# Kernel optimization log

Hardware: AMD Instinct MI355X
Metric: run time of the kernel (lower is better)

The kernel has to match this reference:

```python
import jax, jax.numpy as jnp
import numpy as np

D_K = 64
NEG_INF = -1.0e9

def setup_inputs() -> dict:
    key = jax.random.key(0)
    kq, kk, kv, km = jax.random.split(key, 4)
    B, H, S, D = 2, 16, 2048, D_K
    Q = jax.random.normal(kq, (B, H, S, D), dtype=jnp.float32)
    K = jax.random.normal(kk, (B, H, S, D), dtype=jnp.float32)
    V = jax.random.normal(kv, (B, H, S, D), dtype=jnp.float32)
    # True entries are masked out (torch masked_fill semantics)
    attn_mask = jax.random.randint(km, (B, H, S, S), 0, 2).astype(jnp.bool_)
    return {"Q": Q, "K": K, "V": V, "attn_mask": attn_mask}

def reference(Q, K, V, attn_mask):
    # scores: [B, H, len_q, len_k]
    scale = 1.0 / np.sqrt(D_K).astype(np.float32)
    scores = jnp.einsum('bhqd,bhkd->bhqk', Q, K) * scale
    scores = jnp.where(attn_mask, jnp.float32(NEG_INF), scores)
    attn = jax.nn.softmax(scores, axis=-1)
    prob = jnp.einsum('bhqk,bhkd->bhqd', attn, V)
    return (prob, attn)
```

## Files before the change

### kernel.cpp

```cpp
#include <hip/hip_runtime.h>
#include <hip/hip_bf16.h>

#define S_LEN 2048
#define D_DIM 64
#define QT    64
#define KT    64
#define NTHR  256
#define NKT   (S_LEN / KT)
#define NBLK  1024
#define PROB_ELEMS 4194304LL

typedef float        f32x4  __attribute__((ext_vector_type(4)));
typedef int          i32x4  __attribute__((ext_vector_type(4)));
typedef unsigned int u32x4  __attribute__((ext_vector_type(4)));
typedef short        bf16x8 __attribute__((ext_vector_type(8)));

__device__ __forceinline__ unsigned short f2bf(float f) {
    return __builtin_bit_cast(unsigned short, __float2bfloat16(f));
}
__device__ __forceinline__ int swzc(int row, int ch) {
    return ch ^ ((row ^ (row >> 3)) & 7);
}
__device__ __forceinline__ float4 scale4(float4 v, float s) {
    v.x *= s; v.y *= s; v.z *= s; v.w *= s; return v;
}
__device__ __forceinline__ u32x4 packbf(float4 a, float4 b) {
    u32x4 r;
    r[0] = (unsigned)f2bf(a.x) | ((unsigned)f2bf(a.y) << 16);
    r[1] = (unsigned)f2bf(a.z) | ((unsigned)f2bf(a.w) << 16);
    r[2] = (unsigned)f2bf(b.x) | ((unsigned)f2bf(b.y) << 16);
    r[3] = (unsigned)f2bf(b.z) | ((unsigned)f2bf(b.w) << 16);
    return r;
}
__device__ __forceinline__ unsigned cvtpk(float lo, float hi) {
    unsigned r;
    asm("v_cvt_pk_bf16_f32 %0, %1, %2" : "=v"(r) : "v"(lo), "v"(hi));
    return r;
}
__device__ __forceinline__ void glds16(const unsigned* g, unsigned char* l) {
    __builtin_amdgcn_global_load_lds(
        (const __attribute__((address_space(1))) unsigned*)g,
        (__attribute__((address_space(3))) unsigned*)(void*)l, 16, 0, 0);
}

__global__ void mask_probe_kernel(const unsigned int* __restrict__ m,
                                  int* __restrict__ flag) {
    unsigned int v = m[threadIdx.x];
    unsigned long long ok = __ballot(v <= 1u);
    if (threadIdx.x == 0) *flag = (ok == ~0ULL) ? 1 : 0;
}

#define KPART 524288
#define VPART 65536
__global__ __launch_bounds__(256)
void kv_prep(const float* __restrict__ Kg, const float* __restrict__ Vg,
             unsigned* __restrict__ Kbf, unsigned* __restrict__ Vtb) {
    int tid = blockIdx.x * 256 + threadIdx.x;
    if (tid < KPART) {
        int ch = tid & 7, rowg = tid >> 3;
        const float* src = Kg + (long long)rowg * D_DIM + ch * 8;
        float4 a = *(const float4*)src, b = *(const float4*)(src + 4);
        int bh = rowg >> 11, k = rowg & 2047, kt = k >> 6, row = k & 63;
        unsigned* dst = Kbf + ((unsigned)(bh * NKT + kt) << 11)
                            + row * 32 + swzc(row, ch) * 4;
        *(u32x4*)dst = packbf(a, b);
    } else if (tid < KPART + VPART) {
        int idx = tid - KPART;
        int d = idx & 63, kt = (idx >> 6) & 31, bh = idx >> 11;
        const float* vb = Vg + (long long)(bh * S_LEN + kt * KT) * D_DIM + d;
        unsigned* tile = Vtb + ((unsigned)(bh * NKT + kt) << 11) + d * 32;
        #pragma unroll
        for (int ci = 0; ci < 8; ++ci) {
            u32x4 o;
            #pragma unroll
            for (int s = 0; s < 4; ++s) {
                float lo = vb[(ci * 8 + 2 * s) * D_DIM];
                float hi = vb[(ci * 8 + 2 * s + 1) * D_DIM];
                o[s] = (unsigned)f2bf(lo) | ((unsigned)f2bf(hi) << 16);
            }
            *(u32x4*)(tile + swzc(d, ci) * 4) = o;
        }
    }
}


#define LOAD_MBITS(DST, KTV)                                                \
    { unsigned bz = 0u;                                                     \
      _Pragma("unroll")                                                     \
      for (int n = 0; n < 4; ++n) {                                         \
        unsigned idx = rowoff + (unsigned)((KTV) * KT + n * 16 + 4 * g);    \
        if (mask32) {                                                       \
            i32x4 m4 = *(const i32x4*)(((const int*)maskB) + idx);          \
            bz |= ((m4[0] ? 1u : 0u) | (m4[1] ? 2u : 0u) |                  \
                   (m4[2] ? 4u : 0u) | (m4[3] ? 8u : 0u)) << (n * 4);       \
        } else {                                                            \
            unsigned mb = *(const unsigned*)(maskB + idx);                  \
            bz |= (((mb & 0xffu) ? 1u : 0u) | ((mb & 0xff00u) ? 2u : 0u) |  \
                   ((mb & 0xff0000u) ? 4u : 0u) |                           \
                   ((mb & 0xff000000u) ? 8u : 0u)) << (n * 4);              \
        } }                                                                 \
      (DST) = bz; }

#define LOAD_BITS2(DST, KTV)                                                \
    { if (useWS) (DST) = (unsigned)bitsWS[bitbase + (unsigned)(KTV) * NTHR];\
      else LOAD_MBITS(DST, KTV) }

#define PH1_TILE(KS, BITS)                                                  \
    { unsigned bb = (BITS);                                                 \
      _Pragma("unroll")                                                     \
      for (int n = 0; n < 4; ++n) {                                         \
        int rowk = n * 16 + c;                                              \
        bf16x8 kf0 = *(const bf16x8*)((KS) + rowk * 128 + swzc(rowk, g) * 16);     \
        bf16x8 kf1 = *(const bf16x8*)((KS) + rowk * 128 + swzc(rowk, 4 + g) * 16); \
        f32x4 acc = {0.f, 0.f, 0.f, 0.f};                                   \
        acc = __builtin_amdgcn_mfma_f32_16x16x32_bf16(kf0, qf0, acc, 0, 0, 0); \
        acc = __builtin_amdgcn_mfma_f32_16x16x32_bf16(kf1, qf1, acc, 0, 0, 0); \
        unsigned mb = bb >> (n * 4);                                        \
        psum += (mb & 1u) ? 0.f : __expf(acc[0]);                           \
        psum += (mb & 2u) ? 0.f : __expf(acc[1]);                           \
        psum += (mb & 4u) ? 0.f : __expf(acc[2]);                           \
        psum += (mb & 8u) ? 0.f : __expf(acc[3]);                           \
      } }

#define PH2_TILE(KS, VT, BITS, KTV)                                         \
    { unsigned bb = (BITS);                                                 \
      _Pragma("unroll")                                                     \
      for (int n = 0; n < 4; ++n) {                                         \
        int rowk = n * 16 + c;                                              \
        bf16x8 kf0 = *(const bf16x8*)((KS) + rowk * 128 + swzc(rowk, g) * 16);     \
        bf16x8 kf1 = *(const bf16x8*)((KS) + rowk * 128 + swzc(rowk, 4 + g) * 16); \
        f32x4 acc = {0.f, 0.f, 0.f, 0.f};                                   \
        acc = __builtin_amdgcn_mfma_f32_16x16x32_bf16(kf0, qf0, acc, 0, 0, 0); \
        acc = __builtin_amdgcn_mfma_f32_16x16x32_bf16(kf1, qf1, acc, 0, 0, 0); \
        unsigned mb = bb >> (n * 4);                                        \
        f32x4 ev;                                                           \
        ev[0] = (mb & 1u) ? 0.f : __expf(acc[0]) * rinv;                    \
        ev[1] = (mb & 2u) ? 0.f : __expf(acc[1]) * rinv;                    \
        ev[2] = (mb & 4u) ? 0.f : __expf(acc[2]) * rinv;                    \
        ev[3] = (mb & 8u) ? 0.f : __expf(acc[3]) * rinv;                    \
        unsigned idx0 = rowoff + (unsigned)((KTV) * KT + n * 16 + 4 * g);   \
        __builtin_nontemporal_store(ev, (f32x4*)(attnOut + idx0));          \
        uint2 pkv; pkv.x = cvtpk(ev[0], ev[1]); pkv.y = cvtpk(ev[2], ev[3]);\
        int kloc = n * 16 + 4 * g;                                          \
        *(uint2*)(Ps + ql * 128 + swzc(ql, kloc >> 3) * 16 + (kloc & 7) * 2) = pkv; \
      }                                                                     \
      { bf16x8 pa0 = *(const bf16x8*)(Ps + ql * 128 + swzc(ql, g) * 16);    \
        bf16x8 pa1 = *(const bf16x8*)(Ps + ql * 128 + swzc(ql, 4 + g) * 16);\
        __builtin_amdgcn_s_setprio(1);                                      \
        _Pragma("unroll")                                                   \
        for (int df = 0; df < 4; ++df) {                                    \
            int d = df * 16 + c;                                            \
            bf16x8 vb0 = *(const bf16x8*)((VT) + d * 128 + swzc(d, g) * 16);     \
            bf16x8 vb1 = *(const bf16x8*)((VT) + d * 128 + swzc(d, 4 + g) * 16); \
            pacc[df] = __builtin_amdgcn_mfma_f32_16x16x32_bf16(pa0, vb0, pacc[df], 0, 0, 0); \
            pacc[df] = __builtin_amdgcn_mfma_f32_16x16x32_bf16(pa1, vb1, pacc[df], 0, 0, 0); \
        }                                                                   \
        __builtin_amdgcn_s_setprio(0); } }

__global__ __launch_bounds__(NTHR, 4)
void attn_fused_glds(const float* __restrict__ Qg,
                     const unsigned* __restrict__ Kbf,
                     const unsigned* __restrict__ Vtb,
                     const unsigned char* __restrict__ maskB,
                     const int* __restrict__ flagp,
                     unsigned short* __restrict__ bitsWS, int useWS,
                     float* __restrict__ attnOut, float* __restrict__ probOut) {
    __shared__ unsigned char sm[40960];
    unsigned char* Ks0 = sm;
    unsigned char* Ks1 = sm + 8192;
    unsigned char* Vt0 = sm + 16384;
    unsigned char* Vt1 = sm + 24576;
    unsigned char* Ps  = sm + 32768;

    const int t = threadIdx.x;
    const int lane = t & 63, w = t >> 6, c = lane & 15, g = lane >> 4;

    const int orig = blockIdx.x;
    const int virt = (orig & 7) * 128 + (orig >> 3);
    const int qt = virt & 31, bh = virt >> 5;
    const int mask32 = *flagp;

    const int qrowbase = bh * S_LEN + qt * QT;
    const int ql = w * 16 + c;
    const unsigned rowoff = (unsigned)(qrowbase + ql) * (unsigned)S_LEN;
    const unsigned bitbase = (unsigned)virt * NKT * NTHR + (unsigned)t;
    const unsigned ktile0 = (unsigned)(bh * NKT) << 11;

    const int f0u = t * 4, f1u = (NTHR + t) * 4;
    const int dst0 = (t & ~63) * 16, dst1 = (NTHR + (t & ~63)) * 16;

    #pragma unroll
    for (int i = 0; i < 2; ++i) {
        int flat = i * NTHR + t, row = flat >> 3, ch = flat & 7;
        const float* src = Qg + (qrowbase + row) * D_DIM + ch * 8;
        float4 a = *(const float4*)src, b = *(const float4*)(src + 4);
        *(u32x4*)(Ps + row * 128 + swzc(row, ch) * 16) =
            packbf(scale4(a, 0.125f), scale4(b, 0.125f));
    }
    __syncthreads();
    bf16x8 qf0 = *(const bf16x8*)(Ps + ql * 128 + swzc(ql, g) * 16);
    bf16x8 qf1 = *(const bf16x8*)(Ps + ql * 128 + swzc(ql, 4 + g) * 16);

    float psum = 0.f;
    unsigned bA, bB;
    {
        const unsigned* kp = Kbf + ktile0;
        glds16(kp + f0u, Ks0 + dst0);
        glds16(kp + f1u, Ks0 + dst1);
    }
    LOAD_MBITS(bA, 0)

    for (int j = 0; j < NKT / 2; ++j) {
        const int ktA = 2 * j, ktB = 2 * j + 1;
        __syncthreads();
        {
            const unsigned* kp = Kbf + ktile0 + (unsigned)ktB * 2048;
            glds16(kp + f0u, Ks1 + dst0);
            glds16(kp + f1u, Ks1 + dst1);
        }
        LOAD_MBITS(bB, ktB)
        PH1_TILE(Ks0, bA)
        if (useWS) bitsWS[bitbase + (unsigned)ktA * NTHR] = (unsigned short)bA;

        __syncthreads();
        if (j + 1 < NKT / 2) {
            const unsigned* kp = Kbf + ktile0 + (unsigned)(ktA + 2) * 2048;
            glds16(kp + f0u, Ks0 + dst0);
            glds16(kp + f1u, Ks0 + dst1);
            LOAD_MBITS(bA, ktA + 2)
        }
        PH1_TILE(Ks1, bB)
        if (useWS) bitsWS[bitbase + (unsigned)ktB * NTHR] = (unsigned short)bB;
    }

    float s = psum;
    s += __shfl_xor(s, 16, 64);
    s += __shfl_xor(s, 32, 64);
    const float rinv = 1.0f / s;

    f32x4 pacc[4];
    #pragma unroll
    for (int d = 0; d < 4; ++d) pacc[d] = (f32x4){0.f, 0.f, 0.f, 0.f};

    {
        const unsigned* kp = Kbf + ktile0;
        const unsigned* vp = Vtb + ktile0;
        glds16(kp + f0u, Ks0 + dst0); glds16(kp + f1u, Ks0 + dst1);
        glds16(vp + f0u, Vt0 + dst0); glds16(vp + f1u, Vt0 + dst1);
    }
    LOAD_BITS2(bA, 0)

    for (int j = 0; j < NKT / 2; ++j) {
        const int ktA = 2 * j, ktB = 2 * j + 1;
        __syncthreads();
        {
            const unsigned* kp = Kbf + ktile0 + (unsigned)ktB * 2048;
            const unsigned* vp = Vtb + ktile0 + (unsigned)ktB * 2048;
            glds16(kp + f0u, Ks1 + dst0); glds16(kp + f1u, Ks1 + dst1);
            glds16(vp + f0u, Vt1 + dst0); glds16(vp + f1u, Vt1 + dst1);
        }
        LOAD_BITS2(bB, ktB)
        PH2_TILE(Ks0, Vt0, bA, ktA)

        __syncthreads();
        if (j + 1 < NKT / 2) {
            const unsigned* kp = Kbf + ktile0 + (unsigned)(ktA + 2) * 2048;
            const unsigned* vp = Vtb + ktile0 + (unsigned)(ktA + 2) * 2048;
            glds16(kp + f0u, Ks0 + dst0); glds16(kp + f1u, Ks0 + dst1);
            glds16(vp + f0u, Vt0 + dst0); glds16(vp + f1u, Vt0 + dst1);
            LOAD_BITS2(bA, ktA + 2)
        }
        PH2_TILE(Ks1, Vt1, bB, ktB)
    }

    #pragma unroll
    for (int df = 0; df < 4; ++df)
        #pragma unroll
        for (int r = 0; r < 4; ++r) {
            int qe = w * 16 + g * 4 + r;
            probOut[(long long)(qrowbase + qe) * D_DIM + df * 16 + c] = pacc[df][r];
        }
}

#define LOAD_K(KP, KTV)                                                     \
    { _Pragma("unroll")                                                     \
      for (int i = 0; i < 2; ++i) {                                         \
        int flat = i * NTHR + t, row = flat >> 3, ch = flat & 7;            \
        const float* src = Kg + (kbase + (KTV) * KT + row) * D_DIM + ch * 8;\
        float4 a = *(const float4*)src, b = *(const float4*)(src + 4);      \
        KP[i] = packbf(a, b);                                               \
      } }
#define STAGE_K(KS, KP)                                                     \
    { _Pragma("unroll")                                                     \
      for (int i = 0; i < 2; ++i) {                                         \
        int flat = i * NTHR + t, row = flat >> 3, ch = flat & 7;            \
        *(u32x4*)((KS) + row * 128 + swzc(row, ch) * 16) = KP[i];           \
      } }
#define LOAD_V(VP, KTV)                                                     \
    { const float* src = Vg + (kbase + (KTV) * KT + k0v) * D_DIM + dgv * 8; \
      float4 a = *(const float4*)src, b = *(const float4*)(src + 4);        \
      float4 e4 = *(const float4*)(src + D_DIM);                            \
      float4 f4 = *(const float4*)(src + D_DIM + 4);                        \
      VP[0] = (unsigned)f2bf(a.x) | ((unsigned)f2bf(e4.x) << 16);           \
      VP[1] = (unsigned)f2bf(a.y) | ((unsigned)f2bf(e4.y) << 16);           \
      VP[2] = (unsigned)f2bf(a.z) | ((unsigned)f2bf(e4.z) << 16);           \
      VP[3] = (unsigned)f2bf(a.w) | ((unsigned)f2bf(e4.w) << 16);           \
      VP[4] = (unsigned)f2bf(b.x) | ((unsigned)f2bf(f4.x) << 16);           \
      VP[5] = (unsigned)f2bf(b.y) | ((unsigned)f2bf(f4.y) << 16);           \
      VP[6] = (unsigned)f2bf(b.z) | ((unsigned)f2bf(f4.z) << 16);           \
      VP[7] = (unsigned)f2bf(b.w) | ((unsigned)f2bf(f4.w) << 16); }
#define STAGE_V(VT, VP)                                                     \
    { _Pragma("unroll")                                                     \
      for (int jj = 0; jj < 8; ++jj) {                                      \
        int d = dgv * 8 + jj;                                               \
        *(unsigned*)((VT) + d * 128 + swzc(d, k0v >> 3) * 16 + (k0v & 7) * 2) = VP[jj]; \
      } }

__global__ __launch_bounds__(NTHR, 4)
void attn_fused_reg(const float* __restrict__ Qg, const float* __restrict__ Kg,
                    const float* __restrict__ Vg,
                    const unsigned char* __restrict__ maskB,
                    const int* __restrict__ flagp,
                    unsigned short* __restrict__ bitsWS, int useWS,
                    float* __restrict__ attnOut, float* __restrict__ probOut) {
    __shared__ unsigned char sm[40960];
    unsigned char* Ks0 = sm;
    unsigned char* Ks1 = sm + 8192;
    unsigned char* Vt0 = sm + 16384;
    unsigned char* Vt1 = sm + 24576;
    unsigned char* Ps  = sm + 32768;

    const int t = threadIdx.x;
    const int lane = t & 63, w = t >> 6, c = lane & 15, g = lane >> 4;

    const int orig = blockIdx.x;
    const int virt = (orig & 7) * 128 + (orig >> 3);
    const int qt = virt & 31, bh = virt >> 5;
    const int mask32 = *flagp;

    const int qrowbase = bh * S_LEN + qt * QT;
    const int kbase = bh * S_LEN;
    const int ql = w * 16 + c;
    const unsigned rowoff = (unsigned)(qrowbase + ql) * (unsigned)S_LEN;
    const unsigned bitbase = (unsigned)virt * NKT * NTHR + (unsigned)t;
    const int dgv = t & 7, k0v = (t >> 3) * 2;

    #pragma unroll
    for (int i = 0; i < 2; ++i) {
        int flat = i * NTHR + t, row = flat >> 3, ch = flat & 7;
        const float* src = Qg + (qrowbase + row) * D_DIM + ch * 8;
        float4 a = *(const float4*)src, b = *(const float4*)(src + 4);
        *(u32x4*)(Ps + row * 128 + swzc(row, ch) * 16) =
            packbf(scale4(a, 0.125f), scale4(b, 0.125f));
    }
    __syncthreads();
    bf16x8 qf0 = *(const bf16x8*)(Ps + ql * 128 + swzc(ql, g) * 16);
    bf16x8 qf1 = *(const bf16x8*)(Ps + ql * 128 + swzc(ql, 4 + g) * 16);
    __syncthreads();

    float psum = 0.f;
    u32x4 kpA[2], kpB[2];
    unsigned bA, bB;
    LOAD_K(kpA, 0)
    LOAD_MBITS(bA, 0)

    for (int j = 0; j < NKT / 2; ++j) {
        const int ktA = 2 * j, ktB = 2 * j + 1;
        STAGE_K(Ks0, kpA)
        LOAD_K(kpB, ktB)
        LOAD_MBITS(bB, ktB)
        __syncthreads();
        PH1_TILE(Ks0, bA)
        if (useWS) bitsWS[bitbase + (unsigned)ktA * NTHR] = (unsigned short)bA;
        STAGE_K(Ks1, kpB)
        if (j + 1 < NKT / 2) {
            LOAD_K(kpA, ktA + 2)
            LOAD_MBITS(bA, ktA + 2)
        }
        __syncthreads();
        PH1_TILE(Ks1, bB)
        if (useWS) bitsWS[bitbase + (unsigned)ktB * NTHR] = (unsigned short)bB;
    }

    float s = psum;
    s += __shfl_xor(s, 16, 64);
    s += __shfl_xor(s, 32, 64);
    const float rinv = 1.0f / s;

    f32x4 pacc[4];
    #pragma unroll
    for (int d = 0; d < 4; ++d) pacc[d] = (f32x4){0.f, 0.f, 0.f, 0.f};

    unsigned vpA[8], vpB[8];
    LOAD_K(kpA, 0)
    LOAD_V(vpA, 0)
    LOAD_BITS2(bA, 0)
    __syncthreads();

    for (int j = 0; j < NKT / 2; ++j) {
        const int ktA = 2 * j, ktB = 2 * j + 1;
        STAGE_K(Ks0, kpA)
        STAGE_V(Vt0, vpA)
        LOAD_K(kpB, ktB)
        LOAD_V(vpB, ktB)
        LOAD_BITS2(bB, ktB)
        __syncthreads();
        PH2_TILE(Ks0, Vt0, bA, ktA)
        STAGE_K(Ks1, kpB)
        STAGE_V(Vt1, vpB)
        if (j + 1 < NKT / 2) {
            LOAD_K(kpA, ktA + 2)
            LOAD_V(vpA, ktA + 2)
            LOAD_BITS2(bA, ktA + 2)
        }
        __syncthreads();
        PH2_TILE(Ks1, Vt1, bB, ktB)
    }

    #pragma unroll
    for (int df = 0; df < 4; ++df)
        #pragma unroll
        for (int r = 0; r < 4; ++r) {
            int qe = w * 16 + g * 4 + r;
            probOut[(long long)(qrowbase + qe) * D_DIM + df * 16 + c] = pacc[df][r];
        }
}

extern "C" void kernel_launch(void* const* d_in, const int* in_sizes, int n_in,
                              void* d_out, int out_size, void* d_ws, size_t ws_size,
                              hipStream_t stream) {
    const float* Q = (const float*)d_in[0];
    const float* K = (const float*)d_in[1];
    const float* V = (const float*)d_in[2];
    const unsigned char* mask = (const unsigned char*)d_in[3];

    float* prob = (float*)d_out;
    float* attn = (float*)d_out + PROB_ELEMS;

    const size_t bits_bytes = (size_t)NBLK * NKT * NTHR * 2ull;
    const size_t kbf_bytes  = 8388608ull;
    int* flag = (int*)d_ws;
    unsigned short* bitsWS = (unsigned short*)((char*)d_ws + 256);
    unsigned* Kbf = (unsigned*)((char*)d_ws + 256 + bits_bytes);
    unsigned* Vtb = (unsigned*)((char*)d_ws + 256 + bits_bytes + kbf_bytes);

    const int useWS   = (ws_size >= 256 + bits_bytes) ? 1 : 0;
    const int usePrep = (ws_size >= 256 + bits_bytes + 2 * kbf_bytes) ? 1 : 0;

    mask_probe_kernel<<<1, 64, 0, stream>>>((const unsigned int*)mask, flag);
    if (usePrep) {
        kv_prep<<<(KPART + VPART) / 256, 256, 0, stream>>>(K, V, Kbf, Vtb);
        attn_fused_glds<<<NBLK, NTHR, 0, stream>>>(Q, Kbf, Vtb, mask, flag,
                                                   bitsWS, useWS, attn, prob);
    } else {
        attn_fused_reg<<<NBLK, NTHR, 0, stream>>>(Q, K, V, mask, flag,
                                                  bitsWS, useWS, attn, prob);
    }
}
```

Before: 365.3 us.

## Prepack K/V into MFMA fragment layout and load directly to registers

The prep kernel now writes K and V in per-lane MFMA fragment order, so the main kernel loads operands straight from global memory into registers. This removes the LDS staging through global_load_lds and most __syncthreads. Phase 1 also prefetches the raw mask a tile ahead. Register pressure goes up, occupancy drops from 4 to 3 waves per SIMD, and all four waves in a block now read the same K/V fragments redundantly from global/L2 instead of sharing them in LDS.

```diff
diff --git a/kernel.cpp b/kernel.cpp
--- a/kernel.cpp
+++ b/kernel.cpp
@@ -37,11 +37,7 @@
     asm("v_cvt_pk_bf16_f32 %0, %1, %2" : "=v"(r) : "v"(lo), "v"(hi));
     return r;
 }
-__device__ __forceinline__ void glds16(const unsigned* g, unsigned char* l) {
-    __builtin_amdgcn_global_load_lds(
-        (const __attribute__((address_space(1))) unsigned*)g,
-        (__attribute__((address_space(3))) unsigned*)(void*)l, 16, 0, 0);
-}
+#define BC8(x) __builtin_bit_cast(bf16x8, (x))
 
 __global__ void mask_probe_kernel(const unsigned int* __restrict__ m,
                                   int* __restrict__ flag) {
@@ -50,60 +46,244 @@
     if (threadIdx.x == 0) *flag = (ok == ~0ULL) ? 1 : 0;
 }
 
-#define KPART 524288
-#define VPART 65536
+#define KFRAG_T 524288
+#define VFRAG_T 65536
 __global__ __launch_bounds__(256)
-void kv_prep(const float* __restrict__ Kg, const float* __restrict__ Vg,
-             unsigned* __restrict__ Kbf, unsigned* __restrict__ Vtb) {
+void kv_prep_frag(const float* __restrict__ Kg, const float* __restrict__ Vg,
+                  unsigned* __restrict__ Kf, unsigned* __restrict__ Vf) {
     int tid = blockIdx.x * 256 + threadIdx.x;
-    if (tid < KPART) {
-        int ch = tid & 7, rowg = tid >> 3;
-        const float* src = Kg + (long long)rowg * D_DIM + ch * 8;
+    if (tid < KFRAG_T) {
+        int l = tid & 63, f = (tid >> 6) & 1, n = (tid >> 7) & 3;
+        int kt = (tid >> 9) & 31, bh = tid >> 14;
+        int c = l & 15, g = l >> 4;
+        const float* src = Kg + (long long)(bh * S_LEN + kt * KT + n * 16 + c) * D_DIM
+                              + f * 32 + g * 8;
         float4 a = *(const float4*)src, b = *(const float4*)(src + 4);
-        int bh = rowg >> 11, k = rowg & 2047, kt = k >> 6, row = k & 63;
-        unsigned* dst = Kbf + ((unsigned)(bh * NKT + kt) << 11)
-                            + row * 32 + swzc(row, ch) * 4;
+        unsigned* dst = Kf + ((unsigned)(bh * NKT + kt) << 11)
+                           + (unsigned)((n * 2 + f) * 64 + l) * 4u;
         *(u32x4*)dst = packbf(a, b);
-    } else if (tid < KPART + VPART) {
-        int idx = tid - KPART;
-        int d = idx & 63, kt = (idx >> 6) & 31, bh = idx >> 11;
-        const float* vb = Vg + (long long)(bh * S_LEN + kt * KT) * D_DIM + d;
-        unsigned* tile = Vtb + ((unsigned)(bh * NKT + kt) << 11) + d * 32;
+    } else if (tid < KFRAG_T + VFRAG_T) {
+        int idx = tid - KFRAG_T;
+        int l = idx & 63, kt = (idx >> 6) & 31, bh = idx >> 11;
+        int c = l & 15, g = l >> 4;
+        const float* vb = Vg + (long long)(bh * S_LEN + kt * KT) * D_DIM;
+        unsigned* tile = Vf + ((unsigned)(bh * NKT + kt) << 11);
         #pragma unroll
-        for (int ci = 0; ci < 8; ++ci) {
-            u32x4 o;
+        for (int kb = 0; kb < 2; ++kb)
             #pragma unroll
-            for (int s = 0; s < 4; ++s) {
-                float lo = vb[(ci * 8 + 2 * s) * D_DIM];
-                float hi = vb[(ci * 8 + 2 * s + 1) * D_DIM];
-                o[s] = (unsigned)f2bf(lo) | ((unsigned)f2bf(hi) << 16);
+            for (int df = 0; df < 4; ++df) {
+                u32x4 o;
+                #pragma unroll
+                for (int s = 0; s < 4; ++s) {
+                    int k0 = kb * 32 + g * 8 + 2 * s;
+                    float lo = vb[k0 * D_DIM + df * 16 + c];
+                    float hi = vb[(k0 + 1) * D_DIM + df * 16 + c];
+                    o[s] = (unsigned)f2bf(lo) | ((unsigned)f2bf(hi) << 16);
+                }
+                *(u32x4*)(tile + (unsigned)((kb * 4 + df) * 64 + l) * 4u) = o;
             }
-            *(u32x4*)(tile + swzc(d, ci) * 4) = o;
-        }
-    }
-}
-
+    }
+}
+
+#define LOAD_KFRAG(DST, KTV)                                                \
+    { const u32x4* p_ = (const u32x4*)(Kf + fbase + (unsigned)(KTV) * 2048u) + lane; \
+      _Pragma("unroll")                                                     \
+      for (int i_ = 0; i_ < 8; ++i_) DST[i_] = p_[i_ * 64]; }
+
+#define LOAD_VFRAG(DST, KTV)                                                \
+    { const u32x4* p_ = (const u32x4*)(Vf + fbase + (unsigned)(KTV) * 2048u) + lane; \
+      _Pragma("unroll")                                                     \
+      for (int i_ = 0; i_ < 8; ++i_) DST[i_] = p_[i_ * 64]; }
+
+#define LOAD_M4(DST, KTV)                                                   \
+    { _Pragma("unroll")                                                     \
+      for (int n_ = 0; n_ < 4; ++n_)                                        \
+        DST[n_] = *(const i32x4*)(maskI + rowoff + (unsigned)((KTV) * KT + n_ * 16 + 4 * g)); }
+
+#define BITS_FROM_M4(DST, M)                                                \
+    { unsigned bz_ = 0u;                                                    \
+      _Pragma("unroll")                                                     \
+      for (int n_ = 0; n_ < 4; ++n_)                                        \
+        bz_ |= ((M[n_][0] ? 1u : 0u) | (M[n_][1] ? 2u : 0u) |               \
+                (M[n_][2] ? 4u : 0u) | (M[n_][3] ? 8u : 0u)) << (n_ * 4);   \
+      (DST) = bz_; }
 
 #define LOAD_MBITS(DST, KTV)                                                \
-    { unsigned bz = 0u;                                                     \
-      _Pragma("unroll")                                                     \
-      for (int n = 0; n < 4; ++n) {                                         \
-        unsigned idx = rowoff + (unsigned)((KTV) * KT + n * 16 + 4 * g);    \
+    { unsigned bz_ = 0u;                                                    \
+      _Pragma("unroll")                                                     \
+      for (int n_ = 0; n_ < 4; ++n_) {                                      \
+        unsigned idx_ = rowoff + (unsigned)((KTV) * KT + n_ * 16 + 4 * g);  \
         if (mask32) {                                                       \
-            i32x4 m4 = *(const i32x4*)(((const int*)maskB) + idx);          \
-            bz |= ((m4[0] ? 1u : 0u) | (m4[1] ? 2u : 0u) |                  \
-                   (m4[2] ? 4u : 0u) | (m4[3] ? 8u : 0u)) << (n * 4);       \
+            i32x4 m4_ = *(const i32x4*)(maskI + idx_);                      \
+            bz_ |= ((m4_[0] ? 1u : 0u) | (m4_[1] ? 2u : 0u) |               \
+                    (m4_[2] ? 4u : 0u) | (m4_[3] ? 8u : 0u)) << (n_ * 4);   \
         } else {                                                            \
-            unsigned mb = *(const unsigned*)(maskB + idx);                  \
-            bz |= (((mb & 0xffu) ? 1u : 0u) | ((mb & 0xff00u) ? 2u : 0u) |  \
-                   ((mb & 0xff0000u) ? 4u : 0u) |                           \
-                   ((mb & 0xff000000u) ? 8u : 0u)) << (n * 4);              \
+            unsigned mb_ = *(const unsigned*)(maskB + idx_);                \
+            bz_ |= (((mb_ & 0xffu) ? 1u : 0u) | ((mb_ & 0xff00u) ? 2u : 0u) | \
+                    ((mb_ & 0xff0000u) ? 4u : 0u) |                         \
+                    ((mb_ & 0xff000000u) ? 8u : 0u)) << (n_ * 4);           \
         } }                                                                 \
-      (DST) = bz; }
+      (DST) = bz_; }
 
 #define LOAD_BITS2(DST, KTV)                                                \
     { if (useWS) (DST) = (unsigned)bitsWS[bitbase + (unsigned)(KTV) * NTHR];\
       else LOAD_MBITS(DST, KTV) }
+
+#define QK_FRAG(KC, ACC)                                                    \
+    { _Pragma("unroll")                                                     \
+      for (int n_ = 0; n_ < 4; ++n_) {                                      \
+        f32x4 a_ = {0.f, 0.f, 0.f, 0.f};                                    \
+        a_ = __builtin_amdgcn_mfma_f32_16x16x32_bf16(BC8(KC[2*n_]),   qf0, a_, 0, 0, 0); \
+        a_ = __builtin_amdgcn_mfma_f32_16x16x32_bf16(BC8(KC[2*n_+1]), qf1, a_, 0, 0, 0); \
+        ACC[n_] = a_; } }
+
+#define PH1_FRAG(KC, BITS)                                                  \
+    { unsigned bb_ = (BITS);                                                \
+      _Pragma("unroll")                                                     \
+      for (int n_ = 0; n_ < 4; ++n_) {                                      \
+        f32x4 a_ = {0.f, 0.f, 0.f, 0.f};                                    \
+        a_ = __builtin_amdgcn_mfma_f32_16x16x32_bf16(BC8(KC[2*n_]),   qf0, a_, 0, 0, 0); \
+        a_ = __builtin_amdgcn_mfma_f32_16x16x32_bf16(BC8(KC[2*n_+1]), qf1, a_, 0, 0, 0); \
+        unsigned mb_ = bb_ >> (n_ * 4);                                     \
+        float e0_ = (mb_ & 1u) ? 0.f : __expf(a_[0]);                       \
+        float e1_ = (mb_ & 2u) ? 0.f : __expf(a_[1]);                       \
+        float e2_ = (mb_ & 4u) ? 0.f : __expf(a_[2]);                       \
+        float e3_ = (mb_ & 8u) ? 0.f : __expf(a_[3]);                       \
+        psum += (e0_ + e1_) + (e2_ + e3_); } }
+
+#define SM_P(ACC, BITS, KTV)                                                \
+    { unsigned bb_ = (BITS);                                                \
+      _Pragma("unroll")                                                     \
+      for (int n_ = 0; n_ < 4; ++n_) {                                      \
+        f32x4 a_ = ACC[n_]; unsigned mb_ = bb_ >> (n_ * 4);                 \
+        f32x4 ev_;                                                          \
+        ev_[0] = (mb_ & 1u) ? 0.f : __expf(a_[0]) * rinv;                   \
+        ev_[1] = (mb_ & 2u) ? 0.f : __expf(a_[1]) * rinv;                   \
+        ev_[2] = (mb_ & 4u) ? 0.f : __expf(a_[2]) * rinv;                   \
+        ev_[3] = (mb_ & 8u) ? 0.f : __expf(a_[3]) * rinv;                   \
+        unsigned idx0_ = rowoff + (unsigned)((KTV) * KT + n_ * 16 + 4 * g); \
+        __builtin_nontemporal_store(ev_, (f32x4*)(attnOut + idx0_));        \
+        uint2 pk_; pk_.x = cvtpk(ev_[0], ev_[1]); pk_.y = cvtpk(ev_[2], ev_[3]); \
+        int kloc_ = n_ * 16 + 4 * g;                                        \
+        *(uint2*)(Ps + ql * 128 + swzc(ql, kloc_ >> 3) * 16 + (kloc_ & 7) * 2) = pk_; } }
+
+#define PV_FRAG(VC)                                                         \
+    { bf16x8 pa0_ = *(const bf16x8*)(Ps + ql * 128 + swzc(ql, g) * 16);     \
+      bf16x8 pa1_ = *(const bf16x8*)(Ps + ql * 128 + swzc(ql, 4 + g) * 16); \
+      __builtin_amdgcn_s_setprio(1);                                        \
+      _Pragma("unroll")                                                     \
+      for (int df_ = 0; df_ < 4; ++df_) {                                   \
+        pacc[df_] = __builtin_amdgcn_mfma_f32_16x16x32_bf16(pa0_, BC8(VC[df_]),     pacc[df_], 0, 0, 0); \
+        pacc[df_] = __builtin_amdgcn_mfma_f32_16x16x32_bf16(pa1_, BC8(VC[4 + df_]), pacc[df_], 0, 0, 0); } \
+      __builtin_amdgcn_s_setprio(0); }
+
+__global__ __launch_bounds__(NTHR, 3)
+void attn_fused_frag(const float* __restrict__ Qg,
+                     const unsigned* __restrict__ Kf,
+                     const unsigned* __restrict__ Vf,
+                     const unsigned char* __restrict__ maskB,
+                     const int* __restrict__ flagp,
+                     unsigned short* __restrict__ bitsWS, int useWS,
+                     float* __restrict__ attnOut, float* __restrict__ probOut) {
+    __shared__ unsigned char Ps[8192];
+
+    const int t = threadIdx.x;
+    const int lane = t & 63, w = t >> 6, c = lane & 15, g = lane >> 4;
+
+    const int orig = blockIdx.x;
+    const int virt = (orig & 7) * 128 + (orig >> 3);
+    const int qt = virt & 31, bh = virt >> 5;
+    const int mask32 = *flagp;
+    const int* maskI = (const int*)maskB;
+
+    const int qrowbase = bh * S_LEN + qt * QT;
+    const int ql = w * 16 + c;
+    const unsigned rowoff = (unsigned)(qrowbase + ql) * (unsigned)S_LEN;
+    const unsigned bitbase = (unsigned)virt * NKT * NTHR + (unsigned)t;
+    const unsigned fbase = (unsigned)(bh * NKT) << 11;
+
+    #pragma unroll
+    for (int i = 0; i < 2; ++i) {
+        int flat = i * NTHR + t, row = flat >> 3, ch = flat & 7;
+        const float* src = Qg + (qrowbase + row) * D_DIM + ch * 8;
+        float4 a = *(const float4*)src, b = *(const float4*)(src + 4);
+        *(u32x4*)(Ps + row * 128 + swzc(row, ch) * 16) =
+            packbf(scale4(a, 0.125f), scale4(b, 0.125f));
+    }
+    __syncthreads();
+    bf16x8 qf0 = *(const bf16x8*)(Ps + ql * 128 + swzc(ql, g) * 16);
+    bf16x8 qf1 = *(const bf16x8*)(Ps + ql * 128 + swzc(ql, 4 + g) * 16);
+
+    float psum = 0.f;
+    {
+        u32x4 kA[8], kB[8];
+        i32x4 mA[4], mB[4];
+        unsigned bA, bB;
+        LOAD_KFRAG(kA, 0)
+        if (mask32) { LOAD_M4(mA, 0) }
+
+        for (int j = 0; j < NKT / 2; ++j) {
+            const int ktA = 2 * j, ktB = 2 * j + 1;
+            LOAD_KFRAG(kB, ktB)
+            if (mask32) { LOAD_M4(mB, ktB) BITS_FROM_M4(bA, mA) }
+            else        { LOAD_MBITS(bA, ktA) }
+            PH1_FRAG(kA, bA)
+            if (useWS) bitsWS[bitbase + (unsigned)ktA * NTHR] = (unsigned short)bA;
+
+            if (j + 1 < NKT / 2) {
+                LOAD_KFRAG(kA, ktA + 2)
+                if (mask32) { LOAD_M4(mA, ktA + 2) }
+            }
+            if (mask32) { BITS_FROM_M4(bB, mB) }
+            else        { LOAD_MBITS(bB, ktB) }
+            PH1_FRAG(kB, bB)
+            if (useWS) bitsWS[bitbase + (unsigned)ktB * NTHR] = (unsigned short)bB;
+        }
+    }
+    float s = psum;
+    s += __shfl_xor(s, 16, 64);
+    s += __shfl_xor(s, 32, 64);
+    const float rinv = 1.0f / s;
+
+    f32x4 pacc[4];
+    #pragma unroll
+    for (int d = 0; d < 4; ++d) pacc[d] = (f32x4){0.f, 0.f, 0.f, 0.f};
+
+    {
+        u32x4 kA[8], kB[8], vA[8], vB[8];
+        f32x4 accA[4], accB[4];
+        unsigned bA, bB;
+        LOAD_KFRAG(kA, 0)
+        LOAD_BITS2(bA, 0)
+
+        for (int j = 0; j < NKT / 2; ++j) {
+            const int ktA = 2 * j, ktB = 2 * j + 1;
+            LOAD_KFRAG(kB, ktB)
+            LOAD_BITS2(bB, ktB)
+            QK_FRAG(kA, accA)
+            LOAD_VFRAG(vA, ktA)
+            SM_P(accA, bA, ktA)
+            PV_FRAG(vA)
+
+            if (j + 1 < NKT / 2) {
+                LOAD_KFRAG(kA, ktA + 2)
+                LOAD_BITS2(bA, ktA + 2)
+            }
+            QK_FRAG(kB, accB)
+            LOAD_VFRAG(vB, ktB)
+            SM_P(accB, bB, ktB)
+            PV_FRAG(vB)
+        }
+    }
+
+    #pragma unroll
+    for (int df = 0; df < 4; ++df)
+        #pragma unroll
+        for (int r = 0; r < 4; ++r) {
+            int qe = w * 16 + g * 4 + r;
+            probOut[(long long)(qrowbase + qe) * D_DIM + df * 16 + c] = pacc[df][r];
+        }
+}
 
 #define PH1_TILE(KS, BITS)                                                  \
     { unsigned bb = (BITS);                                                 \
@@ -146,7 +326,6 @@
       }                                                                     \
       { bf16x8 pa0 = *(const bf16x8*)(Ps + ql * 128 + swzc(ql, g) * 16);    \
         bf16x8 pa1 = *(const bf16x8*)(Ps + ql * 128 + swzc(ql, 4 + g) * 16);\
-        __builtin_amdgcn_s_setprio(1);                                      \
         _Pragma("unroll")                                                   \
         for (int df = 0; df < 4; ++df) {                                    \
             int d = df * 16 + c;                                            \
@@ -154,133 +333,7 @@
             bf16x8 vb1 = *(const bf16x8*)((VT) + d * 128 + swzc(d, 4 + g) * 16); \
             pacc[df] = __builtin_amdgcn_mfma_f32_16x16x32_bf16(pa0, vb0, pacc[df], 0, 0, 0); \
             pacc[df] = __builtin_amdgcn_mfma_f32_16x16x32_bf16(pa1, vb1, pacc[df], 0, 0, 0); \
-        }                                                                   \
-        __builtin_amdgcn_s_setprio(0); } }
-
-__global__ __launch_bounds__(NTHR, 4)
-void attn_fused_glds(const float* __restrict__ Qg,
-                     const unsigned* __restrict__ Kbf,
-                     const unsigned* __restrict__ Vtb,
-                     const unsigned char* __restrict__ maskB,
-                     const int* __restrict__ flagp,
-                     unsigned short* __restrict__ bitsWS, int useWS,
-                     float* __restrict__ attnOut, float* __restrict__ probOut) {
-    __shared__ unsigned char sm[40960];
-    unsigned char* Ks0 = sm;
-    unsigned char* Ks1 = sm + 8192;
-    unsigned char* Vt0 = sm + 16384;
-    unsigned char* Vt1 = sm + 24576;
-    unsigned char* Ps  = sm + 32768;
-
-    const int t = threadIdx.x;
-    const int lane = t & 63, w = t >> 6, c = lane & 15, g = lane >> 4;
-
-    const int orig = blockIdx.x;
-    const int virt = (orig & 7) * 128 + (orig >> 3);
-    const int qt = virt & 31, bh = virt >> 5;
-    const int mask32 = *flagp;
-
-    const int qrowbase = bh * S_LEN + qt * QT;
-    const int ql = w * 16 + c;
-    const unsigned rowoff = (unsigned)(qrowbase + ql) * (unsigned)S_LEN;
-    const unsigned bitbase = (unsigned)virt * NKT * NTHR + (unsigned)t;
-    const unsigned ktile0 = (unsigned)(bh * NKT) << 11;
-
-    const int f0u = t * 4, f1u = (NTHR + t) * 4;
-    const int dst0 = (t & ~63) * 16, dst1 = (NTHR + (t & ~63)) * 16;
-
-    #pragma unroll
-    for (int i = 0; i < 2; ++i) {
-        int flat = i * NTHR + t, row = flat >> 3, ch = flat & 7;
-        const float* src = Qg + (qrowbase + row) * D_DIM + ch * 8;
-        float4 a = *(const float4*)src, b = *(const float4*)(src + 4);
-        *(u32x4*)(Ps + row * 128 + swzc(row, ch) * 16) =
-            packbf(scale4(a, 0.125f), scale4(b, 0.125f));
-    }
-    __syncthreads();
-    bf16x8 qf0 = *(const bf16x8*)(Ps + ql * 128 + swzc(ql, g) * 16);
-    bf16x8 qf1 = *(const bf16x8*)(Ps + ql * 128 + swzc(ql, 4 + g) * 16);
-
-    float psum = 0.f;
-    unsigned bA, bB;
-    {
-        const unsigned* kp = Kbf + ktile0;
-        glds16(kp + f0u, Ks0 + dst0);
-        glds16(kp + f1u, Ks0 + dst1);
-    }
-    LOAD_MBITS(bA, 0)
-
-    for (int j = 0; j < NKT / 2; ++j) {
-        const int ktA = 2 * j, ktB = 2 * j + 1;
-        __syncthreads();
-        {
-            const unsigned* kp = Kbf + ktile0 + (unsigned)ktB * 2048;
-            glds16(kp + f0u, Ks1 + dst0);
-            glds16(kp + f1u, Ks1 + dst1);
-        }
-        LOAD_MBITS(bB, ktB)
-        PH1_TILE(Ks0, bA)
-        if (useWS) bitsWS[bitbase + (unsigned)ktA * NTHR] = (unsigned short)bA;
-
-        __syncthreads();
-        if (j + 1 < NKT / 2) {
-            const unsigned* kp = Kbf + ktile0 + (unsigned)(ktA + 2) * 2048;
-            glds16(kp + f0u, Ks0 + dst0);
-            glds16(kp + f1u, Ks0 + dst1);
-            LOAD_MBITS(bA, ktA + 2)
-        }
-        PH1_TILE(Ks1, bB)
-        if (useWS) bitsWS[bitbase + (unsigned)ktB * NTHR] = (unsigned short)bB;
-    }
-
-    float s = psum;
-    s += __shfl_xor(s, 16, 64);
-    s += __shfl_xor(s, 32, 64);
-    const float rinv = 1.0f / s;
-
-    f32x4 pacc[4];
-    #pragma unroll
-    for (int d = 0; d < 4; ++d) pacc[d] = (f32x4){0.f, 0.f, 0.f, 0.f};
-
-    {
-        const unsigned* kp = Kbf + ktile0;
-        const unsigned* vp = Vtb + ktile0;
-        glds16(kp + f0u, Ks0 + dst0); glds16(kp + f1u, Ks0 + dst1);
-        glds16(vp + f0u, Vt0 + dst0); glds16(vp + f1u, Vt0 + dst1);
-    }
-    LOAD_BITS2(bA, 0)
-
-    for (int j = 0; j < NKT / 2; ++j) {
-        const int ktA = 2 * j, ktB = 2 * j + 1;
-        __syncthreads();
-        {
-            const unsigned* kp = Kbf + ktile0 + (unsigned)ktB * 2048;
-            const unsigned* vp = Vtb + ktile0 + (unsigned)ktB * 2048;
-            glds16(kp + f0u, Ks1 + dst0); glds16(kp + f1u, Ks1 + dst1);
-            glds16(vp + f0u, Vt1 + dst0); glds16(vp + f1u, Vt1 + dst1);
-        }
-        LOAD_BITS2(bB, ktB)
-        PH2_TILE(Ks0, Vt0, bA, ktA)
-
-        __syncthreads();
-        if (j + 1 < NKT / 2) {
-            const unsigned* kp = Kbf + ktile0 + (unsigned)(ktA + 2) * 2048;
-            const unsigned* vp = Vtb + ktile0 + (unsigned)(ktA + 2) * 2048;
-            glds16(kp + f0u, Ks0 + dst0); glds16(kp + f1u, Ks0 + dst1);
-            glds16(vp + f0u, Vt0 + dst0); glds16(vp + f1u, Vt0 + dst1);
-            LOAD_BITS2(bA, ktA + 2)
-        }
-        PH2_TILE(Ks1, Vt1, bB, ktB)
-    }
-
-    #pragma unroll
-    for (int df = 0; df < 4; ++df)
-        #pragma unroll
-        for (int r = 0; r < 4; ++r) {
-            int qe = w * 16 + g * 4 + r;
-            probOut[(long long)(qrowbase + qe) * D_DIM + df * 16 + c] = pacc[df][r];
-        }
-}
+        } } }
 
 #define LOAD_K(KP, KTV)                                                     \
     { _Pragma("unroll")                                                     \
@@ -332,11 +385,14 @@
 
     const int t = threadIdx.x;
     const int lane = t & 63, w = t >> 6, c = lane & 15, g = lane >> 4;
+    (void)lane;
 
     const int orig = blockIdx.x;
     const int virt = (orig & 7) * 128 + (orig >> 3);
     const int qt = virt & 31, bh = virt >> 5;
     const int mask32 = *flagp;
+    const int* maskI = (const int*)maskB;
+    (void)maskI;
 
     const int qrowbase = bh * S_LEN + qt * QT;
     const int kbase = bh * S_LEN;
@@ -441,16 +497,16 @@
     const size_t kbf_bytes  = 8388608ull;
     int* flag = (int*)d_ws;
     unsigned short* bitsWS = (unsigned short*)((char*)d_ws + 256);
-    unsigned* Kbf = (unsigned*)((char*)d_ws + 256 + bits_bytes);
-    unsigned* Vtb = (unsigned*)((char*)d_ws + 256 + bits_bytes + kbf_bytes);
+    unsigned* Kf = (unsigned*)((char*)d_ws + 256 + bits_bytes);
+    unsigned* Vf = (unsigned*)((char*)d_ws + 256 + bits_bytes + kbf_bytes);
 
     const int useWS   = (ws_size >= 256 + bits_bytes) ? 1 : 0;
     const int usePrep = (ws_size >= 256 + bits_bytes + 2 * kbf_bytes) ? 1 : 0;
 
     mask_probe_kernel<<<1, 64, 0, stream>>>((const unsigned int*)mask, flag);
     if (usePrep) {
-        kv_prep<<<(KPART + VPART) / 256, 256, 0, stream>>>(K, V, Kbf, Vtb);
-        attn_fused_glds<<<NBLK, NTHR, 0, stream>>>(Q, Kbf, Vtb, mask, flag,
+        kv_prep_frag<<<(KFRAG_T + VFRAG_T) / 256, 256, 0, stream>>>(K, V, Kf, Vf);
+        attn_fused_frag<<<NBLK, NTHR, 0, stream>>>(Q, Kf, Vf, mask, flag,
                                                    bitsWS, useWS, attn, prob);
     } else {
         attn_fused_reg<<<NBLK, NTHR, 0, stream>>>(Q, K, V, mask, flag,
```

Result: slower. 394.3 us (+7.9%).
